# Optimization experiments

Hardware: AMD Instinct MI355X
Metric: run time of the kernel (lower is better)

## Reference

```python
import jax, jax.numpy as jnp
import numpy as np

EPS = 1e-05
RMS_EPS = 1e-06


def activation_quant(x, num_bits=8):
    # per-token (last-dim) abs-max int8 fake quant, computed in fp32
    qn = -(2 ** (num_bits - 1))
    qp = 2 ** (num_bits - 1) - 1
    xf = x.astype(jnp.float32)
    s = qp / jnp.clip(jnp.max(jnp.abs(xf), axis=-1, keepdims=True), EPS, None)
    return (jnp.clip(jnp.round(xf * s), qn, qp) / s).astype(x.dtype)


def weight_quant(w):
    # full-tensor abs-mean ternary fake quant
    wf = w.astype(jnp.float32)
    s = 1.0 / jnp.clip(jnp.mean(jnp.abs(wf)), EPS, None)
    return (jnp.clip(jnp.round(wf * s), -1.0, 1.0) / s).astype(w.dtype)


def bit_linear(x, w):
    # STE wrappers (identity in forward value, straight-through in grad)
    qx = x + jax.lax.stop_gradient(activation_quant(x) - x)
    qw = w + jax.lax.stop_gradient(weight_quant(w) - w)
    return jnp.einsum('bsh,oh->bso', qx, qw)


def rms_norm(x, weight, eps=RMS_EPS):
    xf = x.astype(jnp.float32)
    var = jnp.mean(xf * xf, axis=-1, keepdims=True)
    return weight * (xf * jax.lax.rsqrt(var + eps)).astype(x.dtype)


def setup_inputs() -> dict:
    key = jax.random.key(0)
    k1, k2, k3, k4 = jax.random.split(key, 4)
    B, S, H, I = 2, 2048, 2048, 8192
    scale = 1.0 / np.sqrt(H)
    return {
        'x': jax.random.normal(k1, (B, S, H), dtype=jnp.float32),
        'w_gate': jax.random.normal(k2, (I, H), dtype=jnp.float32) * scale,
        'w_up': jax.random.normal(k3, (I, H), dtype=jnp.float32) * scale,
        'w_down': jax.random.normal(k4, (H, I), dtype=jnp.float32) * (1.0 / np.sqrt(I)),
        'ln_weight': jnp.ones((I,), dtype=jnp.float32),
    }


def reference(x, w_gate, w_up, w_down, ln_weight):
    h = jax.nn.silu(bit_linear(x, w_gate)) * bit_linear(x, w_up)
    h = rms_norm(h, ln_weight)
    return bit_linear(h, w_down)
```

## Files before the change

kernel.cpp:

```cpp
#include <hip/hip_runtime.h>
#include <stdint.h>

typedef int v4i __attribute__((ext_vector_type(4)));

#define TOKENS 4096
#define HDIM   2048
#define IDIM   8192
#define WN     16777216
#define NBLK   512
#define BANDP  5e-7f

static __device__ __forceinline__ void gload_lds16(const void* g, void* l) {
  __builtin_amdgcn_global_load_lds(
      (const __attribute__((address_space(1))) void*)(unsigned long long)(uintptr_t)g,
      (__attribute__((address_space(3))) void*)(unsigned)(uintptr_t)l,
      16, 0, 0);
}

static __device__ __forceinline__ double wsum64d(double v) {
#pragma unroll
  for (int m = 32; m; m >>= 1) v += __shfl_xor(v, m, 64);
  return v;
}
static __device__ __forceinline__ double wmax64d(double v) {
#pragma unroll
  for (int m = 32; m; m >>= 1) v = fmax(v, __shfl_xor(v, m, 64));
  return v;
}
static __device__ __forceinline__ float wmax64f(float v) {
#pragma unroll
  for (int m = 32; m; m >>= 1) v = fmaxf(v, __shfl_xor(v, m, 64));
  return v;
}

static __device__ __forceinline__ int q8f(float v, float s, float lo, float hi) {
  float p = v * s;
  return (int)fminf(fmaxf(rintf(p), lo), hi);
}
static __device__ __forceinline__ uint32_t packq_f(float4 v, float s) {
  int a = q8f(v.x, s, -128.f, 127.f);
  int b = q8f(v.y, s, -128.f, 127.f);
  int c = q8f(v.z, s, -128.f, 127.f);
  int d = q8f(v.w, s, -128.f, 127.f);
  return (uint32_t)((a & 255) | ((b & 255) << 8) | ((c & 255) << 16) | ((d & 255) << 24));
}

__global__ __launch_bounds__(256) void wsum_leaf(const float* __restrict__ wg,
                                                 const float* __restrict__ wu,
                                                 const float* __restrict__ wd,
                                                 float* __restrict__ part) {
  const float* w = blockIdx.y == 0 ? wg : (blockIdx.y == 1 ? wu : wd);
  int tid = threadIdx.x;
  const float4* w4 = (const float4*)w;
  size_t base4 = ((size_t)blockIdx.x * 256 + tid) * 32;
  float4 p = w4[base4], q = w4[base4 + 1];
  float r0 = fabsf(p.x), r1 = fabsf(p.y), r2 = fabsf(p.z), r3 = fabsf(p.w);
  float r4 = fabsf(q.x), r5 = fabsf(q.y), r6 = fabsf(q.z), r7 = fabsf(q.w);
  for (int i = 2; i < 32; i += 2) {
    float4 a = w4[base4 + i], b = w4[base4 + i + 1];
    r0 += fabsf(a.x); r1 += fabsf(a.y); r2 += fabsf(a.z); r3 += fabsf(a.w);
    r4 += fabsf(b.x); r5 += fabsf(b.y); r6 += fabsf(b.z); r7 += fabsf(b.w);
  }
  float leaf = ((r0 + r1) + (r2 + r3)) + ((r4 + r5) + (r6 + r7));
  __shared__ float A[256], B[256];
  A[tid] = leaf;
  __syncthreads();
  float* src = A; float* dst = B;
  for (int n = 128; n >= 1; n >>= 1) {
    if (tid < n) dst[tid] = src[2 * tid] + src[2 * tid + 1];
    __syncthreads();
    float* t = src; src = dst; dst = t;
  }
  if (tid == 0) part[blockIdx.y * NBLK + blockIdx.x] = src[0];
}

__global__ __launch_bounds__(256) void wsum_final(const float* __restrict__ part,
                                                  float* __restrict__ wsc) {
  int t = blockIdx.x, tid = threadIdx.x;
  __shared__ float A[512], B[256];
  A[tid] = part[t * NBLK + tid];
  A[tid + 256] = part[t * NBLK + tid + 256];
  __syncthreads();
  float* src = A; float* dst = B;
  for (int n = 256; n >= 1; n >>= 1) {
    if (tid < n) dst[tid] = src[2 * tid] + src[2 * tid + 1];
    __syncthreads();
    float* tmp = src; src = dst; dst = tmp;
  }
  if (tid == 0) {
    float mean32 = src[0] / (float)WN;
    float m32 = fmaxf(mean32, 1e-5f);
    float s32 = 1.0f / m32;
    wsc[t] = s32;
    wsc[3 + t] = 1.0f / s32;
  }
}

__global__ __launch_bounds__(256) void wquant_kernel(const float* __restrict__ wg,
                                                     const float* __restrict__ wu,
                                                     const float* __restrict__ wd,
                                                     const float* __restrict__ wsc,
                                                     int8_t* __restrict__ qg,
                                                     int8_t* __restrict__ qu,
                                                     int8_t* __restrict__ qd) {
  int t = blockIdx.y;
  const float* w = t == 0 ? wg : (t == 1 ? wu : wd);
  int8_t* q = t == 0 ? qg : (t == 1 ? qu : qd);
  float s32 = wsc[t];
  const float4* w4 = (const float4*)w;
  uint32_t* q4 = (uint32_t*)q;
  const int n4 = WN / 4;
  for (int i = blockIdx.x * 256 + threadIdx.x; i < n4; i += gridDim.x * 256) {
    float4 v = w4[i];
    float vv[4] = {v.x, v.y, v.z, v.w};
    int o[4];
#pragma unroll
    for (int j = 0; j < 4; ++j) {
      float pf = fabsf(vv[j]) * s32;
      int q2 = 2 * (int)fminf(rintf(pf), 1.0f);
      if (fabsf(pf - 0.5f) < BANDP) q2 = 1;
      o[j] = (vv[j] < 0.0f) ? -q2 : q2;
    }
    q4[i] = (uint32_t)((o[0] & 255) | ((o[1] & 255) << 8) |
                       ((o[2] & 255) << 16) | ((o[3] & 255) << 24));
  }
}

__global__ __launch_bounds__(256) void xquant_kernel(const float* __restrict__ x,
                                                     int8_t* __restrict__ qx,
                                                     double* __restrict__ axd) {
  int row = blockIdx.x, tid = threadIdx.x;
  const float4* xr = (const float4*)(x + (size_t)row * HDIM);
  float4 v0 = xr[tid], v1 = xr[tid + 256];
  float m = fmaxf(fmaxf(fmaxf(fabsf(v0.x), fabsf(v0.y)), fmaxf(fabsf(v0.z), fabsf(v0.w))),
                  fmaxf(fmaxf(fabsf(v1.x), fabsf(v1.y)), fmaxf(fabsf(v1.z), fabsf(v1.w))));
  m = wmax64f(m);
  __shared__ float red[4];
  int wid = tid >> 6, lane = tid & 63;
  if (lane == 0) red[wid] = m;
  __syncthreads();
  float mm = fmaxf(fmaxf(red[0], red[1]), fmaxf(red[2], red[3]));
  float c32 = fmaxf(mm, 1e-5f);
  float s32 = 127.0f / c32;
  if (tid == 0) axd[row] = 1.0 / (double)s32;
  uint32_t* q4 = (uint32_t*)(qx + (size_t)row * HDIM);
  q4[tid] = packq_f(v0, s32);
  q4[tid + 256] = packq_f(v1, s32);
}

__global__ __launch_bounds__(512, 4) void gemm1_kernel(const int8_t* __restrict__ qx,
                                                       const int8_t* __restrict__ qg,
                                                       const int8_t* __restrict__ qu,
                                                       const float* __restrict__ wsc,
                                                       const double* __restrict__ axd,
                                                       float* __restrict__ h) {
  extern __shared__ char lds[];
  int tid = threadIdx.x, wid = tid >> 6, lane = tid & 63;
  int l15 = lane & 15, lgp = lane >> 4;
  int wr = wid >> 2, wc = wid & 3;
  int flat = blockIdx.y * 64 + blockIdx.x;
  int xcd = flat & 7, local = flat >> 3;
  int mt = local >> 3, nl = local & 7;
  int m0 = mt * 128, n0 = (xcd * 8 + nl) * 128;
  const int8_t* bA = qx + (size_t)m0 * HDIM;
  const int8_t* bG = qg + (size_t)n0 * HDIM;
  const int8_t* bU = qu + (size_t)n0 * HDIM;

  v4i accg[4][2], accu[4][2];
  v4i vzero = {0, 0, 0, 0};
#pragma unroll
  for (int i = 0; i < 4; ++i)
#pragma unroll
    for (int j = 0; j < 2; ++j) { accg[i][j] = vzero; accu[i][j] = vzero; }

  int aoff[4], goff[2], uoff[2];
#pragma unroll
  for (int i = 0; i < 4; ++i)
    aoff[i] = lgp * 2048 + (wr * 64 + i * 16 + l15) * 16;
#pragma unroll
  for (int i = 0; i < 2; ++i) {
    goff[i] = 8192 + lgp * 2048 + (wc * 32 + i * 16 + l15) * 16;
    uoff[i] = goff[i] + 8192;
  }

  int srow = tid & 127, sslab = tid >> 7;
  const size_t rA = (size_t)srow * HDIM;
  int sdst = sslab * 2048 + srow * 16;

  const int NT = HDIM / 64;
  {
    size_t k0 = (size_t)sslab * 16;
    gload_lds16(bA + rA + k0, lds + sdst);
    gload_lds16(bG + rA + k0, lds + sdst + 8192);
    gload_lds16(bU + rA + k0, lds + sdst + 16384);
    size_t k1 = 64 + (size_t)sslab * 16;
    gload_lds16(bA + rA + k1, lds + 24576 + sdst);
    gload_lds16(bG + rA + k1, lds + 24576 + sdst + 8192);
    gload_lds16(bU + rA + k1, lds + 24576 + sdst + 16384);
  }
  asm volatile("s_waitcnt vmcnt(3)" ::: "memory");
  __builtin_amdgcn_s_barrier();
  __builtin_amdgcn_sched_barrier(0);

  int c0 = 0, c1 = 24576, c2 = 49152;
  for (int t = 0; t < NT; ++t) {
    if (t + 2 < NT) {
      size_t koff = (size_t)(t + 2) * 64 + sslab * 16;
      gload_lds16(bA + rA + koff, lds + c2 + sdst);
      gload_lds16(bG + rA + koff, lds + c2 + sdst + 8192);
      gload_lds16(bU + rA + koff, lds + c2 + sdst + 16384);
    }
    v4i a[4], bg[2], bu[2];
#pragma unroll
    for (int i = 0; i < 4; ++i) a[i] = *(const v4i*)(lds + c0 + aoff[i]);
#pragma unroll
    for (int i = 0; i < 2; ++i) {
      bg[i] = *(const v4i*)(lds + c0 + goff[i]);
      bu[i] = *(const v4i*)(lds + c0 + uoff[i]);
    }
#pragma unroll
    for (int mi = 0; mi < 4; ++mi)
#pragma unroll
      for (int ni = 0; ni < 2; ++ni) {
        accg[mi][ni] = __builtin_amdgcn_mfma_i32_16x16x64_i8(a[mi], bg[ni], accg[mi][ni], 0, 0, 0);
        accu[mi][ni] = __builtin_amdgcn_mfma_i32_16x16x64_i8(a[mi], bu[ni], accu[mi][ni], 0, 0, 0);
      }
    __builtin_amdgcn_sched_barrier(0);
    if (t + 2 < NT)
      asm volatile("s_waitcnt vmcnt(3)" ::: "memory");
    else
      asm volatile("s_waitcnt vmcnt(0)" ::: "memory");
    __builtin_amdgcn_s_barrier();
    __builtin_amdgcn_sched_barrier(0);
    int tmp = c0; c0 = c1; c1 = c2; c2 = tmp;
  }

  double mg = 0.5 * (double)wsc[3 + 0];
  double mu = 0.5 * (double)wsc[3 + 1];
#pragma unroll
  for (int mi = 0; mi < 4; ++mi) {
#pragma unroll
    for (int rg = 0; rg < 4; ++rg) {
      int grow = m0 + wr * 64 + mi * 16 + lgp * 4 + rg;
      double axr = axd[grow];
      double sg = axr * mg, su = axr * mu;
#pragma unroll
      for (int ni = 0; ni < 2; ++ni) {
        int gcol = n0 + wc * 32 + ni * 16 + l15;
        double g = (double)accg[mi][ni][rg] * sg;
        double u = (double)accu[mi][ni][rg] * su;
        double sig = 1.0 / (1.0 + exp(-g));
        h[(size_t)grow * IDIM + gcol] = (float)((g * sig) * u);
      }
    }
  }
}

__global__ __launch_bounds__(256) void hquant_kernel(const float* __restrict__ h,
                                                     const float* __restrict__ lnw,
                                                     double* __restrict__ ahd,
                                                     int8_t* __restrict__ qh) {
  int row = blockIdx.x, tid = threadIdx.x;
  const float4* hr = (const float4*)(h + (size_t)row * IDIM);
  const float4* lw4 = (const float4*)lnw;
  float4 hv[8], wv[8];
  double ssq = 0.0;
#pragma unroll
  for (int i = 0; i < 8; ++i) {
    hv[i] = hr[tid + i * 256];
    wv[i] = lw4[tid + i * 256];
    ssq += (double)hv[i].x * hv[i].x + (double)hv[i].y * hv[i].y +
           (double)hv[i].z * hv[i].z + (double)hv[i].w * hv[i].w;
  }
  ssq = wsum64d(ssq);
  __shared__ double redd[4];
  __shared__ double redm[4];
  int wid = tid >> 6, lane = tid & 63;
  if (lane == 0) redd[wid] = ssq;
  __syncthreads();
  double tot = redd[0] + redd[1] + redd[2] + redd[3];
  double rd = 1.0 / sqrt(tot * (1.0 / (double)IDIM) + 1e-6);
  double mx = 0.0;
#pragma unroll
  for (int i = 0; i < 8; ++i) {
    double y0 = (double)wv[i].x * ((double)hv[i].x * rd);
    double y1 = (double)wv[i].y * ((double)hv[i].y * rd);
    double y2 = (double)wv[i].z * ((double)hv[i].z * rd);
    double y3 = (double)wv[i].w * ((double)hv[i].w * rd);
    mx = fmax(mx, fmax(fmax(fabs(y0), fabs(y1)), fmax(fabs(y2), fabs(y3))));
  }
  mx = wmax64d(mx);
  if (lane == 0) redm[wid] = mx;
  __syncthreads();
  double mm = fmax(fmax(redm[0], redm[1]), fmax(redm[2], redm[3]));
  float c32 = fmaxf((float)mm, 1e-5f);
  float s32 = 127.0f / c32;
  double sd = (double)s32;
  if (tid == 0) ahd[row] = 1.0 / (double)s32;
  uint32_t* q4 = (uint32_t*)(qh + (size_t)row * IDIM);
#pragma unroll
  for (int i = 0; i < 8; ++i) {
    double y0 = (double)wv[i].x * ((double)hv[i].x * rd);
    double y1 = (double)wv[i].y * ((double)hv[i].y * rd);
    double y2 = (double)wv[i].z * ((double)hv[i].z * rd);
    double y3 = (double)wv[i].w * ((double)hv[i].w * rd);
    int a = (int)fmin(fmax(rint(y0 * sd), -128.0), 127.0);
    int b = (int)fmin(fmax(rint(y1 * sd), -128.0), 127.0);
    int c = (int)fmin(fmax(rint(y2 * sd), -128.0), 127.0);
    int d = (int)fmin(fmax(rint(y3 * sd), -128.0), 127.0);
    q4[tid + i * 256] = (uint32_t)((a & 255) | ((b & 255) << 8) | ((c & 255) << 16) | ((d & 255) << 24));
  }
}

__global__ __launch_bounds__(512, 4) void gemm2_kernel(const int8_t* __restrict__ qh,
                                                       const int8_t* __restrict__ qd,
                                                       const float* __restrict__ wsc,
                                                       const double* __restrict__ ahd,
                                                       float* __restrict__ out) {
  extern __shared__ char lds[];
  int tid = threadIdx.x, wid = tid >> 6, lane = tid & 63;
  int l15 = lane & 15, lgp = lane >> 4;
  int wr = wid >> 2, wc = wid & 3;
  int flat = blockIdx.y * 16 + blockIdx.x;
  int xcd = flat & 7, local = flat >> 3;
  int mt = xcd * 4 + (local >> 4), nt = local & 15;
  int m0 = mt * 128, n0 = nt * 128;
  const int8_t* bA = qh + (size_t)m0 * IDIM;
  const int8_t* bB = qd + (size_t)n0 * IDIM;

  v4i acc[4][2];
  v4i vzero = {0, 0, 0, 0};
#pragma unroll
  for (int i = 0; i < 4; ++i)
#pragma unroll
    for (int j = 0; j < 2; ++j) acc[i][j] = vzero;

  int aoff[4], boff[2];
#pragma unroll
  for (int i = 0; i < 4; ++i)
    aoff[i] = lgp * 2048 + (wr * 64 + i * 16 + l15) * 16;
#pragma unroll
  for (int i = 0; i < 2; ++i)
    boff[i] = 8192 + lgp * 2048 + (wc * 32 + i * 16 + l15) * 16;

  int srow = tid & 127, sslab = tid >> 7;
  const size_t rA = (size_t)srow * IDIM;
  int sdst = sslab * 2048 + srow * 16;

  const int NT = IDIM / 64;
  {
    size_t k0 = (size_t)sslab * 16;
    gload_lds16(bA + rA + k0, lds + sdst);
    gload_lds16(bB + rA + k0, lds + sdst + 8192);
    size_t k1 = 64 + (size_t)sslab * 16;
    gload_lds16(bA + rA + k1, lds + 16384 + sdst);
    gload_lds16(bB + rA + k1, lds + 16384 + sdst + 8192);
  }
  asm volatile("s_waitcnt vmcnt(2)" ::: "memory");
  __builtin_amdgcn_s_barrier();
  __builtin_amdgcn_sched_barrier(0);

  int c0 = 0, c1 = 16384, c2 = 32768;
  for (int t = 0; t < NT; ++t) {
    if (t + 2 < NT) {
      size_t koff = (size_t)(t + 2) * 64 + sslab * 16;
      gload_lds16(bA + rA + koff, lds + c2 + sdst);
      gload_lds16(bB + rA + koff, lds + c2 + sdst + 8192);
    }
    v4i a[4], b[2];
#pragma unroll
    for (int i = 0; i < 4; ++i) a[i] = *(const v4i*)(lds + c0 + aoff[i]);
#pragma unroll
    for (int i = 0; i < 2; ++i) b[i] = *(const v4i*)(lds + c0 + boff[i]);
#pragma unroll
    for (int mi = 0; mi < 4; ++mi)
#pragma unroll
      for (int ni = 0; ni < 2; ++ni)
        acc[mi][ni] = __builtin_amdgcn_mfma_i32_16x16x64_i8(a[mi], b[ni], acc[mi][ni], 0, 0, 0);
    __builtin_amdgcn_sched_barrier(0);
    if (t + 2 < NT)
      asm volatile("s_waitcnt vmcnt(2)" ::: "memory");
    else
      asm volatile("s_waitcnt vmcnt(0)" ::: "memory");
    __builtin_amdgcn_s_barrier();
    __builtin_amdgcn_sched_barrier(0);
    int tmp = c0; c0 = c1; c1 = c2; c2 = tmp;
  }

  double md = 0.5 * (double)wsc[3 + 2];
#pragma unroll
  for (int mi = 0; mi < 4; ++mi) {
#pragma unroll
    for (int rg = 0; rg < 4; ++rg) {
      int grow = m0 + wr * 64 + mi * 16 + lgp * 4 + rg;
      double sc = ahd[grow] * md;
#pragma unroll
      for (int ni = 0; ni < 2; ++ni) {
        int gcol = n0 + wc * 32 + ni * 16 + l15;
        out[(size_t)grow * HDIM + gcol] = (float)((double)acc[mi][ni][rg] * sc);
      }
    }
  }
}

extern "C" void kernel_launch(void* const* d_in, const int* in_sizes, int n_in,
                              void* d_out, int out_size, void* d_ws, size_t ws_size,
                              hipStream_t stream) {
  const float* x   = (const float*)d_in[0];
  const float* wg  = (const float*)d_in[1];
  const float* wu  = (const float*)d_in[2];
  const float* wd  = (const float*)d_in[3];
  const float* lnw = (const float*)d_in[4];
  float* out = (float*)d_out;
  char* ws = (char*)d_ws;

  size_t off = 0;
  auto alloc = [&](size_t b) { size_t o = off; off += (b + 255) & ~(size_t)255; return o; };
  size_t o_wsc  = alloc(8 * 4);
  size_t o_part = alloc(3 * NBLK * 4);
  size_t o_axd  = alloc((size_t)TOKENS * 8);
  size_t o_ahd  = alloc((size_t)TOKENS * 8);
  size_t o_qx   = alloc((size_t)TOKENS * HDIM);
  size_t o_qg   = alloc((size_t)IDIM * HDIM);
  size_t o_qu   = alloc((size_t)IDIM * HDIM);
  size_t o_qd   = alloc((size_t)HDIM * IDIM);
  size_t o_h    = alloc((size_t)TOKENS * IDIM * 4);
  (void)ws_size; (void)in_sizes; (void)n_in; (void)out_size; (void)o_qu;

  float* wsc  = (float*)(ws + o_wsc);
  float* part = (float*)(ws + o_part);
  double* axd = (double*)(ws + o_axd);
  double* ahd = (double*)(ws + o_ahd);
  int8_t* qx  = (int8_t*)(ws + o_qx);
  int8_t* qg  = (int8_t*)(ws + o_qg);
  int8_t* qu  = (int8_t*)(ws + o_qu);
  int8_t* qd  = (int8_t*)(ws + o_qd);
  int8_t* qh  = (int8_t*)(ws + o_qg);
  float* h    = (float*)(ws + o_h);

  wsum_leaf<<<dim3(NBLK, 3), 256, 0, stream>>>(wg, wu, wd, part);
  wsum_final<<<3, 256, 0, stream>>>(part, wsc);
  wquant_kernel<<<dim3(1024, 3), 256, 0, stream>>>(wg, wu, wd, wsc, qg, qu, qd);
  xquant_kernel<<<TOKENS, 256, 0, stream>>>(x, qx, axd);
  gemm1_kernel<<<dim3(IDIM / 128, TOKENS / 128), 512, 3 * 24576, stream>>>(qx, qg, qu, wsc, axd, h);
  hquant_kernel<<<TOKENS, 256, 0, stream>>>(h, lnw, ahd, qh);
  gemm2_kernel<<<dim3(HDIM / 128, TOKENS / 128), 512, 3 * 16384, stream>>>(qh, qd, wsc, ahd, out);
}
```

Before: 522.8 us.

## Split int8 GEMM main loops into ping-pong phases with setprio and barriers

Both int8 MFMA main loops (gate/up and down) are restructured into several phases. Each phase issues a few LDS fragment loads and one global-to-LDS prefetch, then runs a group of four MFMAs at raised wave priority (s_setprio). Extra workgroup barriers keep waves in lockstep so memory and matrix work from different waves interleave, following the ping-pong scheduling style. The cost is many more s_barrier instructions per iteration, plus the risk that the forced serialization of LDS reads and MFMAs lowers throughput.

```diff
diff --git a/kernel.cpp b/kernel.cpp
--- a/kernel.cpp
+++ b/kernel.cpp
@@ -9,6 +9,8 @@
 #define WN     16777216
 #define NBLK   512
 #define BANDP  5e-7f
+
+#define MFMA_I8 __builtin_amdgcn_mfma_i32_16x16x64_i8
 
 static __device__ __forceinline__ void gload_lds16(const void* g, void* l) {
   __builtin_amdgcn_global_load_lds(
@@ -204,34 +206,62 @@
 
   int c0 = 0, c1 = 24576, c2 = 49152;
   for (int t = 0; t < NT; ++t) {
-    if (t + 2 < NT) {
-      size_t koff = (size_t)(t + 2) * 64 + sslab * 16;
-      gload_lds16(bA + rA + koff, lds + c2 + sdst);
-      gload_lds16(bG + rA + koff, lds + c2 + sdst + 8192);
-      gload_lds16(bU + rA + koff, lds + c2 + sdst + 16384);
-    }
-    v4i a[4], bg[2], bu[2];
-#pragma unroll
-    for (int i = 0; i < 4; ++i) a[i] = *(const v4i*)(lds + c0 + aoff[i]);
-#pragma unroll
-    for (int i = 0; i < 2; ++i) {
-      bg[i] = *(const v4i*)(lds + c0 + goff[i]);
-      bu[i] = *(const v4i*)(lds + c0 + uoff[i]);
-    }
-#pragma unroll
-    for (int mi = 0; mi < 4; ++mi)
-#pragma unroll
-      for (int ni = 0; ni < 2; ++ni) {
-        accg[mi][ni] = __builtin_amdgcn_mfma_i32_16x16x64_i8(a[mi], bg[ni], accg[mi][ni], 0, 0, 0);
-        accu[mi][ni] = __builtin_amdgcn_mfma_i32_16x16x64_i8(a[mi], bu[ni], accu[mi][ni], 0, 0, 0);
-      }
-    __builtin_amdgcn_sched_barrier(0);
-    if (t + 2 < NT)
+    const bool pf = (t + 2 < NT);
+    size_t koff = (size_t)(t + 2) * 64 + sslab * 16;
+    v4i a0 = *(const v4i*)(lds + c0 + aoff[0]);
+    v4i a1 = *(const v4i*)(lds + c0 + aoff[1]);
+    v4i bg0 = *(const v4i*)(lds + c0 + goff[0]);
+    v4i bg1 = *(const v4i*)(lds + c0 + goff[1]);
+    if (pf) gload_lds16(bA + rA + koff, lds + c2 + sdst);
+    __builtin_amdgcn_s_barrier();
+    asm volatile("s_waitcnt lgkmcnt(0)" ::: "memory");
+    __builtin_amdgcn_sched_barrier(0);
+    __builtin_amdgcn_s_setprio(1);
+    accg[0][0] = MFMA_I8(a0, bg0, accg[0][0], 0, 0, 0);
+    accg[0][1] = MFMA_I8(a0, bg1, accg[0][1], 0, 0, 0);
+    accg[1][0] = MFMA_I8(a1, bg0, accg[1][0], 0, 0, 0);
+    accg[1][1] = MFMA_I8(a1, bg1, accg[1][1], 0, 0, 0);
+    __builtin_amdgcn_s_setprio(0);
+    __builtin_amdgcn_s_barrier();
+    v4i a2 = *(const v4i*)(lds + c0 + aoff[2]);
+    v4i a3 = *(const v4i*)(lds + c0 + aoff[3]);
+    if (pf) gload_lds16(bG + rA + koff, lds + c2 + sdst + 8192);
+    __builtin_amdgcn_s_barrier();
+    asm volatile("s_waitcnt lgkmcnt(0)" ::: "memory");
+    __builtin_amdgcn_sched_barrier(0);
+    __builtin_amdgcn_s_setprio(1);
+    accg[2][0] = MFMA_I8(a2, bg0, accg[2][0], 0, 0, 0);
+    accg[2][1] = MFMA_I8(a2, bg1, accg[2][1], 0, 0, 0);
+    accg[3][0] = MFMA_I8(a3, bg0, accg[3][0], 0, 0, 0);
+    accg[3][1] = MFMA_I8(a3, bg1, accg[3][1], 0, 0, 0);
+    __builtin_amdgcn_s_setprio(0);
+    __builtin_amdgcn_s_barrier();
+    v4i bu0 = *(const v4i*)(lds + c0 + uoff[0]);
+    v4i bu1 = *(const v4i*)(lds + c0 + uoff[1]);
+    if (pf) gload_lds16(bU + rA + koff, lds + c2 + sdst + 16384);
+    __builtin_amdgcn_s_barrier();
+    asm volatile("s_waitcnt lgkmcnt(0)" ::: "memory");
+    __builtin_amdgcn_sched_barrier(0);
+    __builtin_amdgcn_s_setprio(1);
+    accu[0][0] = MFMA_I8(a0, bu0, accu[0][0], 0, 0, 0);
+    accu[0][1] = MFMA_I8(a0, bu1, accu[0][1], 0, 0, 0);
+    accu[1][0] = MFMA_I8(a1, bu0, accu[1][0], 0, 0, 0);
+    accu[1][1] = MFMA_I8(a1, bu1, accu[1][1], 0, 0, 0);
+    __builtin_amdgcn_s_setprio(0);
+    __builtin_amdgcn_s_barrier();
+    if (pf)
       asm volatile("s_waitcnt vmcnt(3)" ::: "memory");
     else
       asm volatile("s_waitcnt vmcnt(0)" ::: "memory");
     __builtin_amdgcn_s_barrier();
     __builtin_amdgcn_sched_barrier(0);
+    __builtin_amdgcn_s_setprio(1);
+    accu[2][0] = MFMA_I8(a2, bu0, accu[2][0], 0, 0, 0);
+    accu[2][1] = MFMA_I8(a2, bu1, accu[2][1], 0, 0, 0);
+    accu[3][0] = MFMA_I8(a3, bu0, accu[3][0], 0, 0, 0);
+    accu[3][1] = MFMA_I8(a3, bu1, accu[3][1], 0, 0, 0);
+    __builtin_amdgcn_s_setprio(0);
+    __builtin_amdgcn_s_barrier();
     int tmp = c0; c0 = c1; c1 = c2; c2 = tmp;
   }
 
@@ -362,28 +392,40 @@
 
   int c0 = 0, c1 = 16384, c2 = 32768;
   for (int t = 0; t < NT; ++t) {
-    if (t + 2 < NT) {
-      size_t koff = (size_t)(t + 2) * 64 + sslab * 16;
-      gload_lds16(bA + rA + koff, lds + c2 + sdst);
-      gload_lds16(bB + rA + koff, lds + c2 + sdst + 8192);
-    }
-    v4i a[4], b[2];
-#pragma unroll
-    for (int i = 0; i < 4; ++i) a[i] = *(const v4i*)(lds + c0 + aoff[i]);
-#pragma unroll
-    for (int i = 0; i < 2; ++i) b[i] = *(const v4i*)(lds + c0 + boff[i]);
-#pragma unroll
-    for (int mi = 0; mi < 4; ++mi)
-#pragma unroll
-      for (int ni = 0; ni < 2; ++ni)
-        acc[mi][ni] = __builtin_amdgcn_mfma_i32_16x16x64_i8(a[mi], b[ni], acc[mi][ni], 0, 0, 0);
-    __builtin_amdgcn_sched_barrier(0);
-    if (t + 2 < NT)
+    const bool pf = (t + 2 < NT);
+    size_t koff = (size_t)(t + 2) * 64 + sslab * 16;
+    v4i a0 = *(const v4i*)(lds + c0 + aoff[0]);
+    v4i a1 = *(const v4i*)(lds + c0 + aoff[1]);
+    v4i b0 = *(const v4i*)(lds + c0 + boff[0]);
+    v4i b1 = *(const v4i*)(lds + c0 + boff[1]);
+    if (pf) gload_lds16(bA + rA + koff, lds + c2 + sdst);
+    __builtin_amdgcn_s_barrier();
+    asm volatile("s_waitcnt lgkmcnt(0)" ::: "memory");
+    __builtin_amdgcn_sched_barrier(0);
+    __builtin_amdgcn_s_setprio(1);
+    acc[0][0] = MFMA_I8(a0, b0, acc[0][0], 0, 0, 0);
+    acc[0][1] = MFMA_I8(a0, b1, acc[0][1], 0, 0, 0);
+    acc[1][0] = MFMA_I8(a1, b0, acc[1][0], 0, 0, 0);
+    acc[1][1] = MFMA_I8(a1, b1, acc[1][1], 0, 0, 0);
+    __builtin_amdgcn_s_setprio(0);
+    __builtin_amdgcn_s_barrier();
+    v4i a2 = *(const v4i*)(lds + c0 + aoff[2]);
+    v4i a3 = *(const v4i*)(lds + c0 + aoff[3]);
+    if (pf) gload_lds16(bB + rA + koff, lds + c2 + sdst + 8192);
+    if (pf)
       asm volatile("s_waitcnt vmcnt(2)" ::: "memory");
     else
       asm volatile("s_waitcnt vmcnt(0)" ::: "memory");
     __builtin_amdgcn_s_barrier();
-    __builtin_amdgcn_sched_barrier(0);
+    asm volatile("s_waitcnt lgkmcnt(0)" ::: "memory");
+    __builtin_amdgcn_sched_barrier(0);
+    __builtin_amdgcn_s_setprio(1);
+    acc[2][0] = MFMA_I8(a2, b0, acc[2][0], 0, 0, 0);
+    acc[2][1] = MFMA_I8(a2, b1, acc[2][1], 0, 0, 0);
+    acc[3][0] = MFMA_I8(a3, b0, acc[3][0], 0, 0, 0);
+    acc[3][1] = MFMA_I8(a3, b1, acc[3][1], 0, 0, 0);
+    __builtin_amdgcn_s_setprio(0);
+    __builtin_amdgcn_s_barrier();
     int tmp = c0; c0 = c1; c1 = c2; c2 = tmp;
   }
 
```

Measured after the change: 495.4 us. 5.2% less time.
